# Performance work log

Measured on AMD Instinct MI355X. Metric: run time of the kernel, lower is better.

The kernel has to match this reference:

```python
import jax, jax.numpy as jnp
import numpy as np

DELTA = 0.1
NEG_INF = -1e30


def setup_inputs() -> dict:
    key = jax.random.key(0)
    k1, k2, k3, k4 = jax.random.split(key, 4)
    Bs, Bt, D, C = 8192, 8192, 64, 10
    return {
        "src_feas": jax.random.normal(k1, (Bs, D), dtype=jnp.float32),
        "src_labels": jax.random.randint(k2, (Bs,), 0, C, dtype=jnp.int32),
        "tgt_feas": jax.random.normal(k3, (Bt, D), dtype=jnp.float32),
        "tgt_logits": jax.random.normal(k4, (Bt, C), dtype=jnp.float32),
    }


def reference(src_feas, src_labels, tgt_feas, tgt_logits):
    # The original builds the explicit list of positive pairs (i_tgt, j_src)
    # where tgt sample i is 'confident' (top1-top2 logit gap >= delta) and
    # src_labels[j] == argmax(tgt_logits[i]).  The [P, P] score matrix it
    # forms is s[k, l] = src_feas[j_k] . tgt_feas[i_l], which only depends on
    # (j_k, i_l), so sum(diag(log_softmax(s))) collapses to a weighted
    # logsumexp over the [Bs, Bt] cross-domain score matrix. Same math,
    # fully vectorized, order-invariant.
    Bs = src_feas.shape[0]
    C = tgt_logits.shape[1]

    top2 = jax.lax.top_k(tgt_logits, 2)[0]                  # [Bt, 2]
    conf = (top2[:, 0] - top2[:, 1]) >= DELTA               # [Bt]
    cls = jnp.argmax(tgt_logits, axis=1)                    # [Bt]

    # per-class count of source samples
    counts = jnp.zeros((C,), jnp.float32).at[src_labels].add(1.0)  # [C]
    # w[i] = multiplicity of tgt sample i in the pair list
    w = jnp.where(conf, counts[cls], 0.0)                   # [Bt]

    M = src_feas @ tgt_feas.T                               # [Bs, Bt]
    logw = jnp.where(w > 0, jnp.log(jnp.maximum(w, 1.0)), NEG_INF)
    # L[j] = log sum over all pairs l of exp(M[j, i_l])
    L = jax.scipy.special.logsumexp(M + logw[None, :], axis=1)  # [Bs]

    pair_mask = conf[None, :] & (src_labels[:, None] == cls[None, :])  # [Bs, Bt]
    nce_sum = jnp.sum(jnp.where(pair_mask, M - L[:, None], 0.0))
    P = jnp.sum(w)                                          # total pair count
    nce = nce_sum / (-1.0 * Bs * P)
    return nce
```

## Files before the change

kernel.cpp:

```cpp
#include <hip/hip_runtime.h>
#include <hip/hip_bf16.h>

#define BSZ 8192
#define BTZ 8192
#define DD 64
#define NC 10
#define SHIFT2 20.0f
#define LN2 0.69314718055994531f
#define LOG2E 1.44269504088896341f

typedef __attribute__((ext_vector_type(8))) short bf16x8;
typedef __attribute__((ext_vector_type(4))) float f32x4;

#if defined(__has_builtin)
#if __has_builtin(__builtin_amdgcn_exp2f)
#define EXP2(x) __builtin_amdgcn_exp2f(x)
#else
#define EXP2(x) exp2f(x)
#endif
#else
#define EXP2(x) exp2f(x)
#endif

__device__ __forceinline__ unsigned short f2bf_rne(float f) {
    unsigned int u = __float_as_uint(f);
    u += 0x7FFFu + ((u >> 16) & 1u);
    return (unsigned short)(u >> 16);
}

__global__ void kA(const float4* __restrict__ src4, const float4* __restrict__ tgt4,
                   const int* __restrict__ labels,
                   ushort4* __restrict__ srcb, ushort4* __restrict__ tgtb,
                   float* __restrict__ cnt_part) {
    __shared__ float hist[NC];
    int t = threadIdx.x;
    int tid = blockIdx.x * 256 + t;
    float4 s = src4[tid];
    ushort4 os;
    os.x = f2bf_rne(s.x * LOG2E); os.y = f2bf_rne(s.y * LOG2E);
    os.z = f2bf_rne(s.z * LOG2E); os.w = f2bf_rne(s.w * LOG2E);
    srcb[tid] = os;
    float4 v = tgt4[tid];
    ushort4 ot; ot.x = f2bf_rne(v.x); ot.y = f2bf_rne(v.y);
    ot.z = f2bf_rne(v.z); ot.w = f2bf_rne(v.w);
    tgtb[tid] = ot;

    if (blockIdx.x < 32) {
        if (t < NC) hist[t] = 0.0f;
        __syncthreads();
        atomicAdd(&hist[labels[tid]], 1.0f);
        __syncthreads();
        if (t < NC) cnt_part[blockIdx.x * NC + t] = hist[t];
    }
}

__global__ void kB(const float* __restrict__ logits,
                   const float* __restrict__ cnt_part,
                   float* __restrict__ colbias, unsigned char* __restrict__ cls8,
                   float* __restrict__ cc_part, float* __restrict__ S) {
    __shared__ float lcnt[NC];
    __shared__ float hist[NC];
    int t = threadIdx.x;
    int i = blockIdx.x * 256 + t;

    if (t < NC) {
        float c = 0.0f;
        #pragma unroll
        for (int b = 0; b < 32; ++b) c += cnt_part[b * NC + t];
        lcnt[t] = c;
        hist[t] = 0.0f;
    }

    float m1 = -3.0e38f, m2 = -3.0e38f; int cls = 0;
    #pragma unroll
    for (int c = 0; c < NC; ++c) {
        float v = logits[i * NC + c];
        if (v > m1) { m2 = m1; m1 = v; cls = c; }
        else if (v > m2) { m2 = v; }
    }
    bool conf = (m1 - m2) >= 0.1f;
    __syncthreads();
    float cnt = lcnt[cls];
    bool live = conf && (cnt > 0.0f);
    colbias[i] = live ? (log2f(cnt) - SHIFT2) : -1.0e30f;
    cls8[i] = live ? (unsigned char)cls : (unsigned char)255;
    S[i] = 0.0f;
    if (conf) atomicAdd(&hist[cls], 1.0f);
    __syncthreads();
    if (t < NC) cc_part[blockIdx.x * NC + t] = hist[t];
}

__global__ __launch_bounds__(256) void kC(const unsigned short* __restrict__ srcb,
                                          const unsigned short* __restrict__ tgtb,
                                          const float* __restrict__ colbias,
                                          const unsigned char* __restrict__ cls8,
                                          const int* __restrict__ labels,
                                          float* __restrict__ S,
                                          float* __restrict__ term1_part) {
    __shared__ float lds[4][64];
    __shared__ float t1red[4];
    int t = threadIdx.x;
    int w = t >> 6;
    int lane = t & 63;
    int l15 = lane & 15;
    int quad = lane >> 4;
    int colchunk = blockIdx.x & 15;
    int rowg = blockIdx.x >> 4;
    int row_base = rowg * 64;

    bf16x8 a[4][2];
    int rl[4][4];
    #pragma unroll
    for (int mb = 0; mb < 4; ++mb) {
        const bf16x8* p = (const bf16x8*)(srcb + (size_t)(row_base + mb * 16 + l15) * DD + quad * 8);
        a[mb][0] = p[0];
        a[mb][1] = p[4];
        #pragma unroll
        for (int r = 0; r < 4; ++r)
            rl[mb][r] = labels[row_base + mb * 16 + quad * 4 + r];
    }

    float rs[4][4];
    #pragma unroll
    for (int mb = 0; mb < 4; ++mb)
        #pragma unroll
        for (int r = 0; r < 4; ++r) rs[mb][r] = 0.0f;
    float t1p = 0.0f;

    int col0 = colchunk * 512 + w * 128;
    #pragma unroll 2
    for (int ct = 0; ct < 8; ++ct) {
        int cb = col0 + ct * 16;
        const bf16x8* q = (const bf16x8*)(tgtb + (size_t)(cb + l15) * DD + quad * 8);
        bf16x8 b0 = q[0];
        bf16x8 b1 = q[4];
        float cb2 = colbias[cb + l15];
        int ccls = (int)cls8[cb + l15];
        #pragma unroll
        for (int mb = 0; mb < 4; ++mb) {
            f32x4 acc = {cb2, cb2, cb2, cb2};
            acc = __builtin_amdgcn_mfma_f32_16x16x32_bf16(a[mb][0], b0, acc, 0, 0, 0);
            acc = __builtin_amdgcn_mfma_f32_16x16x32_bf16(a[mb][1], b1, acc, 0, 0, 0);
            #pragma unroll
            for (int r = 0; r < 4; ++r) {
                float e = acc[r];
                rs[mb][r] += EXP2(e);
                t1p += (ccls == rl[mb][r]) ? (e - cb2) : 0.0f;
            }
        }
    }

    #pragma unroll
    for (int mb = 0; mb < 4; ++mb) {
        #pragma unroll
        for (int r = 0; r < 4; ++r) {
            float v = rs[mb][r];
            v += __shfl_xor(v, 1);
            v += __shfl_xor(v, 2);
            v += __shfl_xor(v, 4);
            v += __shfl_xor(v, 8);
            if (l15 == 0) lds[w][mb * 16 + quad * 4 + r] = v;
        }
    }
    float tv = t1p;
    #pragma unroll
    for (int m = 1; m < 64; m <<= 1) tv += __shfl_xor(tv, m);
    if (lane == 0) t1red[w] = tv;
    __syncthreads();
    if (t < 64)
        atomicAdd(&S[row_base + t], lds[0][t] + lds[1][t] + lds[2][t] + lds[3][t]);
    if (t == 128)
        term1_part[blockIdx.x] = t1red[0] + t1red[1] + t1red[2] + t1red[3];
}

__global__ void kD(const float* __restrict__ S, const int* __restrict__ labels,
                   const float* __restrict__ cnt_part, const float* __restrict__ cc_part,
                   const float* __restrict__ term1_part,
                   float* __restrict__ out) {
    __shared__ float counts[NC], cc[NC];
    int t = threadIdx.x;
    if (t < NC) {
        float c0 = 0.0f, c1 = 0.0f;
        #pragma unroll
        for (int b = 0; b < 32; ++b) { c0 += cnt_part[b * NC + t]; c1 += cc_part[b * NC + t]; }
        counts[t] = c0; cc[t] = c1;
    }
    __syncthreads();

    float termL = 0.0f, term1 = 0.0f, P = 0.0f;
    for (int j = t; j < BSZ; j += 256) {
        float L = (log2f(S[j]) + SHIFT2) * LN2;
        termL += cc[labels[j]] * L;
    }
    for (int o = t; o < 2048; o += 256) term1 += term1_part[o];
    if (t < NC) P = counts[t] * cc[t];

    __shared__ float redL[4], red1[4], redP[4];
    int w = t >> 6, lane = t & 63;
    float v1 = termL, v2 = term1, v3 = P;
    #pragma unroll
    for (int m = 1; m < 64; m <<= 1) {
        v1 += __shfl_xor(v1, m);
        v2 += __shfl_xor(v2, m);
        v3 += __shfl_xor(v3, m);
    }
    if (lane == 0) { redL[w] = v1; red1[w] = v2; redP[w] = v3; }
    __syncthreads();
    if (t == 0) {
        float tl = redL[0] + redL[1] + redL[2] + redL[3];
        float t1 = (red1[0] + red1[1] + red1[2] + red1[3]) * LN2;
        float p  = redP[0] + redP[1] + redP[2] + redP[3];
        out[0] = (t1 - tl) / (-(float)BSZ * p);
    }
}

extern "C" void kernel_launch(void* const* d_in, const int* in_sizes, int n_in,
                              void* d_out, int out_size, void* d_ws, size_t ws_size,
                              hipStream_t stream) {
    const float* src    = (const float*)d_in[0];
    const int*   labels = (const int*)d_in[1];
    const float* tgt    = (const float*)d_in[2];
    const float* logits = (const float*)d_in[3];

    char* ws = (char*)d_ws;
    float* S          = (float*)(ws + 0);
    float* cnt_part   = (float*)(ws + 32768);
    float* cc_part    = (float*)(ws + 34048);
    float* term1_part = (float*)(ws + 35328);
    float* colbias    = (float*)(ws + 65536);
    unsigned char* cls8 = (unsigned char*)(ws + 98304);
    unsigned short* srcb = (unsigned short*)(ws + 131072);
    unsigned short* tgtb = (unsigned short*)(ws + 131072 + 1048576);

    kA<<<512, 256, 0, stream>>>((const float4*)src, (const float4*)tgt, labels,
                                (ushort4*)srcb, (ushort4*)tgtb, cnt_part);
    kB<<<32, 256, 0, stream>>>(logits, cnt_part, colbias, cls8, cc_part, S);
    kC<<<2048, 256, 0, stream>>>(srcb, tgtb, colbias, cls8, labels, S, term1_part);
    kD<<<1, 256, 0, stream>>>(S, labels, cnt_part, cc_part, term1_part, (float*)d_out);
}
```

Before: 110.2 us.

## Compute positive-pair term via per-class target sums and fuse kernels into two

```diff
diff --git a/kernel.cpp b/kernel.cpp
--- a/kernel.cpp
+++ b/kernel.cpp
@@ -8,6 +8,7 @@
 #define SHIFT2 20.0f
 #define LN2 0.69314718055994531f
 #define LOG2E 1.44269504088896341f
+#define NEG_BIG -1.0e30f
 
 typedef __attribute__((ext_vector_type(8))) short bf16x8;
 typedef __attribute__((ext_vector_type(4))) float f32x4;
@@ -28,48 +29,51 @@
     return (unsigned short)(u >> 16);
 }
 
-__global__ void kA(const float4* __restrict__ src4, const float4* __restrict__ tgt4,
-                   const int* __restrict__ labels,
-                   ushort4* __restrict__ srcb, ushort4* __restrict__ tgtb,
-                   float* __restrict__ cnt_part) {
+__global__ __launch_bounds__(256) void kAB(const float4* __restrict__ src4,
+                                           const float4* __restrict__ tgt4,
+                                           const int* __restrict__ labels,
+                                           const float* __restrict__ logits,
+                                           const float* __restrict__ tgtf,
+                                           ushort4* __restrict__ srcb,
+                                           ushort4* __restrict__ tgtb,
+                                           float* __restrict__ S,
+                                           float* __restrict__ colbias,
+                                           float* __restrict__ cc_part,
+                                           float* __restrict__ counts_g,
+                                           float* __restrict__ accs,
+                                           int* __restrict__ ctrl,
+                                           float* __restrict__ T_part) {
     __shared__ float hist[NC];
+    __shared__ float chist[NC];
+    __shared__ unsigned char cls_l[256];
+    __shared__ float red[4 * 640];
+
     int t = threadIdx.x;
-    int tid = blockIdx.x * 256 + t;
-    float4 s = src4[tid];
-    ushort4 os;
-    os.x = f2bf_rne(s.x * LOG2E); os.y = f2bf_rne(s.y * LOG2E);
-    os.z = f2bf_rne(s.z * LOG2E); os.w = f2bf_rne(s.w * LOG2E);
-    srcb[tid] = os;
-    float4 v = tgt4[tid];
-    ushort4 ot; ot.x = f2bf_rne(v.x); ot.y = f2bf_rne(v.y);
-    ot.z = f2bf_rne(v.z); ot.w = f2bf_rne(v.w);
-    tgtb[tid] = ot;
-
-    if (blockIdx.x < 32) {
-        if (t < NC) hist[t] = 0.0f;
-        __syncthreads();
-        atomicAdd(&hist[labels[tid]], 1.0f);
-        __syncthreads();
-        if (t < NC) cnt_part[blockIdx.x * NC + t] = hist[t];
-    }
-}
-
-__global__ void kB(const float* __restrict__ logits,
-                   const float* __restrict__ cnt_part,
-                   float* __restrict__ colbias, unsigned char* __restrict__ cls8,
-                   float* __restrict__ cc_part, float* __restrict__ S) {
-    __shared__ float lcnt[NC];
-    __shared__ float hist[NC];
-    int t = threadIdx.x;
-    int i = blockIdx.x * 256 + t;
-
-    if (t < NC) {
-        float c = 0.0f;
-        #pragma unroll
-        for (int b = 0; b < 32; ++b) c += cnt_part[b * NC + t];
-        lcnt[t] = c;
-        hist[t] = 0.0f;
-    }
+    int b = blockIdx.x;
+
+    if (b < 512) {
+        int tid = b * 256 + t;
+        float4 s = src4[tid];
+        ushort4 os;
+        os.x = f2bf_rne(s.x * LOG2E); os.y = f2bf_rne(s.y * LOG2E);
+        os.z = f2bf_rne(s.z * LOG2E); os.w = f2bf_rne(s.w * LOG2E);
+        srcb[tid] = os;
+        float4 v = tgt4[tid];
+        ushort4 ot;
+        ot.x = f2bf_rne(v.x); ot.y = f2bf_rne(v.y);
+        ot.z = f2bf_rne(v.z); ot.w = f2bf_rne(v.w);
+        tgtb[tid] = ot;
+        return;
+    }
+
+    int lb = b - 512;
+    int i = lb * 256 + t;
+
+    if (t < NC) { hist[t] = 0.0f; chist[t] = 0.0f; }
+    __syncthreads();
+
+    #pragma unroll
+    for (int it = 0; it < 32; ++it) atomicAdd(&hist[labels[it * 256 + t]], 1.0f);
 
     float m1 = -3.0e38f, m2 = -3.0e38f; int cls = 0;
     #pragma unroll
@@ -80,25 +84,71 @@
     }
     bool conf = (m1 - m2) >= 0.1f;
     __syncthreads();
-    float cnt = lcnt[cls];
+
+    float cnt = hist[cls];
     bool live = conf && (cnt > 0.0f);
-    colbias[i] = live ? (log2f(cnt) - SHIFT2) : -1.0e30f;
-    cls8[i] = live ? (unsigned char)cls : (unsigned char)255;
+    colbias[i] = live ? (log2f(cnt) - SHIFT2) : NEG_BIG;
     S[i] = 0.0f;
-    if (conf) atomicAdd(&hist[cls], 1.0f);
-    __syncthreads();
-    if (t < NC) cc_part[blockIdx.x * NC + t] = hist[t];
+    cls_l[t] = live ? (unsigned char)cls : (unsigned char)255;
+    if (conf) atomicAdd(&chist[cls], 1.0f);
+    __syncthreads();
+
+    if (t < NC) cc_part[lb * NC + t] = chist[t];
+    if (lb == 0) {
+        if (t < NC) counts_g[t] = hist[t];
+        if (t < 2) accs[t] = 0.0f;
+        if (t < 129) ctrl[t] = 0;
+    }
+
+    int w = t >> 6, lane = t & 63;
+    float Ta[NC];
+    #pragma unroll
+    for (int c = 0; c < NC; ++c) Ta[c] = 0.0f;
+    int I0 = lb * 256;
+    for (int k = 0; k < 64; ++k) {
+        int li = w * 64 + k;
+        int c = (int)cls_l[li];
+        c = __builtin_amdgcn_readfirstlane(c);
+        if (c < NC) {
+            float v = tgtf[(size_t)(I0 + li) * DD + lane];
+            if      (c == 0) Ta[0] += v;
+            else if (c == 1) Ta[1] += v;
+            else if (c == 2) Ta[2] += v;
+            else if (c == 3) Ta[3] += v;
+            else if (c == 4) Ta[4] += v;
+            else if (c == 5) Ta[5] += v;
+            else if (c == 6) Ta[6] += v;
+            else if (c == 7) Ta[7] += v;
+            else if (c == 8) Ta[8] += v;
+            else             Ta[9] += v;
+        }
+    }
+    #pragma unroll
+    for (int c = 0; c < NC; ++c) red[w * 640 + c * 64 + lane] = Ta[c];
+    __syncthreads();
+    for (int idx = t; idx < 640; idx += 256)
+        T_part[lb * 640 + idx] =
+            red[idx] + red[640 + idx] + red[1280 + idx] + red[1920 + idx];
 }
 
-__global__ __launch_bounds__(256) void kC(const unsigned short* __restrict__ srcb,
-                                          const unsigned short* __restrict__ tgtb,
-                                          const float* __restrict__ colbias,
-                                          const unsigned char* __restrict__ cls8,
-                                          const int* __restrict__ labels,
-                                          float* __restrict__ S,
-                                          float* __restrict__ term1_part) {
+__global__ __launch_bounds__(256) void kCD(const unsigned short* __restrict__ srcb,
+                                           const unsigned short* __restrict__ tgtb,
+                                           const float* __restrict__ colbias,
+                                           const float* __restrict__ srcf,
+                                           const int* __restrict__ labels,
+                                           const float* __restrict__ cc_part,
+                                           const float* __restrict__ counts_g,
+                                           const float* __restrict__ T_part,
+                                           float* __restrict__ S,
+                                           float* __restrict__ accs,
+                                           int* __restrict__ ctrl,
+                                           float* __restrict__ out) {
     __shared__ float lds[4][64];
+    __shared__ float Tl[660];
     __shared__ float t1red[4];
+    __shared__ float ccl[NC];
+    __shared__ int flag1, flag2;
+
     int t = threadIdx.x;
     int w = t >> 6;
     int lane = t & 63;
@@ -109,15 +159,11 @@
     int row_base = rowg * 64;
 
     bf16x8 a[4][2];
-    int rl[4][4];
     #pragma unroll
     for (int mb = 0; mb < 4; ++mb) {
         const bf16x8* p = (const bf16x8*)(srcb + (size_t)(row_base + mb * 16 + l15) * DD + quad * 8);
         a[mb][0] = p[0];
         a[mb][1] = p[4];
-        #pragma unroll
-        for (int r = 0; r < 4; ++r)
-            rl[mb][r] = labels[row_base + mb * 16 + quad * 4 + r];
     }
 
     float rs[4][4];
@@ -125,29 +171,33 @@
     for (int mb = 0; mb < 4; ++mb)
         #pragma unroll
         for (int r = 0; r < 4; ++r) rs[mb][r] = 0.0f;
-    float t1p = 0.0f;
 
     int col0 = colchunk * 512 + w * 128;
+    const bf16x8* q0 = (const bf16x8*)(tgtb + (size_t)(col0 + l15) * DD + quad * 8);
+    bf16x8 b0 = q0[0];
+    bf16x8 b1 = q0[4];
+    float cb2 = colbias[col0 + l15];
+
     #pragma unroll 2
     for (int ct = 0; ct < 8; ++ct) {
-        int cb = col0 + ct * 16;
-        const bf16x8* q = (const bf16x8*)(tgtb + (size_t)(cb + l15) * DD + quad * 8);
-        bf16x8 b0 = q[0];
-        bf16x8 b1 = q[4];
-        float cb2 = colbias[cb + l15];
-        int ccls = (int)cls8[cb + l15];
+        bf16x8 nb0 = b0, nb1 = b1;
+        float ncb2 = cb2;
+        if (ct < 7) {
+            int cb = col0 + (ct + 1) * 16;
+            const bf16x8* qn = (const bf16x8*)(tgtb + (size_t)(cb + l15) * DD + quad * 8);
+            nb0 = qn[0];
+            nb1 = qn[4];
+            ncb2 = colbias[cb + l15];
+        }
         #pragma unroll
         for (int mb = 0; mb < 4; ++mb) {
             f32x4 acc = {cb2, cb2, cb2, cb2};
             acc = __builtin_amdgcn_mfma_f32_16x16x32_bf16(a[mb][0], b0, acc, 0, 0, 0);
             acc = __builtin_amdgcn_mfma_f32_16x16x32_bf16(a[mb][1], b1, acc, 0, 0, 0);
             #pragma unroll
-            for (int r = 0; r < 4; ++r) {
-                float e = acc[r];
-                rs[mb][r] += EXP2(e);
-                t1p += (ccls == rl[mb][r]) ? (e - cb2) : 0.0f;
-            }
-        }
+            for (int r = 0; r < 4; ++r) rs[mb][r] += EXP2(acc[r]);
+        }
+        b0 = nb0; b1 = nb1; cb2 = ncb2;
     }
 
     #pragma unroll
@@ -162,55 +212,74 @@
             if (l15 == 0) lds[w][mb * 16 + quad * 4 + r] = v;
         }
     }
-    float tv = t1p;
-    #pragma unroll
-    for (int m = 1; m < 64; m <<= 1) tv += __shfl_xor(tv, m);
-    if (lane == 0) t1red[w] = tv;
     __syncthreads();
     if (t < 64)
         atomicAdd(&S[row_base + t], lds[0][t] + lds[1][t] + lds[2][t] + lds[3][t]);
-    if (t == 128)
-        term1_part[blockIdx.x] = t1red[0] + t1red[1] + t1red[2] + t1red[3];
-}
-
-__global__ void kD(const float* __restrict__ S, const int* __restrict__ labels,
-                   const float* __restrict__ cnt_part, const float* __restrict__ cc_part,
-                   const float* __restrict__ term1_part,
-                   float* __restrict__ out) {
-    __shared__ float counts[NC], cc[NC];
-    int t = threadIdx.x;
+
+    if (colchunk == 0) {
+        for (int idx = t; idx < 640; idx += 256) {
+            float sm = 0.0f;
+            #pragma unroll
+            for (int p = 0; p < 32; ++p) sm += T_part[p * 640 + idx];
+            Tl[(idx >> 6) * 66 + (idx & 63)] = sm;
+        }
+        __syncthreads();
+        int r = t >> 2, dq = t & 3;
+        int lab = labels[row_base + r];
+        const float4* sp = (const float4*)(srcf + (size_t)(row_base + r) * DD + dq * 16);
+        float part = 0.0f;
+        #pragma unroll
+        for (int j4 = 0; j4 < 4; ++j4) {
+            float4 sv = sp[j4];
+            int tb = lab * 66 + dq * 16 + j4 * 4;
+            part += sv.x * Tl[tb] + sv.y * Tl[tb + 1] + sv.z * Tl[tb + 2] + sv.w * Tl[tb + 3];
+        }
+        #pragma unroll
+        for (int m = 1; m < 64; m <<= 1) part += __shfl_xor(part, m);
+        if (lane == 0) t1red[w] = part;
+        __syncthreads();
+        if (t == 0) atomicAdd(&accs[1], t1red[0] + t1red[1] + t1red[2] + t1red[3]);
+    }
+
+    __syncthreads();
+    __threadfence();
+    if (t == 0) { int old = atomicAdd(&ctrl[rowg], 1); flag1 = (old == 15) ? 1 : 0; }
+    __syncthreads();
+    if (!flag1) return;
+
+    __threadfence();
     if (t < NC) {
-        float c0 = 0.0f, c1 = 0.0f;
-        #pragma unroll
-        for (int b = 0; b < 32; ++b) { c0 += cnt_part[b * NC + t]; c1 += cc_part[b * NC + t]; }
-        counts[t] = c0; cc[t] = c1;
-    }
-    __syncthreads();
-
-    float termL = 0.0f, term1 = 0.0f, P = 0.0f;
-    for (int j = t; j < BSZ; j += 256) {
-        float L = (log2f(S[j]) + SHIFT2) * LN2;
-        termL += cc[labels[j]] * L;
-    }
-    for (int o = t; o < 2048; o += 256) term1 += term1_part[o];
-    if (t < NC) P = counts[t] * cc[t];
-
-    __shared__ float redL[4], red1[4], redP[4];
-    int w = t >> 6, lane = t & 63;
-    float v1 = termL, v2 = term1, v3 = P;
-    #pragma unroll
-    for (int m = 1; m < 64; m <<= 1) {
-        v1 += __shfl_xor(v1, m);
-        v2 += __shfl_xor(v2, m);
-        v3 += __shfl_xor(v3, m);
-    }
-    if (lane == 0) { redL[w] = v1; red1[w] = v2; redP[w] = v3; }
-    __syncthreads();
+        float s = 0.0f;
+        #pragma unroll
+        for (int p = 0; p < 32; ++p) s += cc_part[p * NC + t];
+        ccl[t] = s;
+    }
+    __syncthreads();
+    float val = 0.0f;
+    if (t < 64) {
+        float s = __hip_atomic_load(&S[row_base + t], __ATOMIC_RELAXED, __HIP_MEMORY_SCOPE_AGENT);
+        float L = (log2f(s) + SHIFT2) * LN2;
+        val = ccl[labels[row_base + t]] * L;
+    }
+    if (w == 0) {
+        #pragma unroll
+        for (int m = 1; m < 64; m <<= 1) val += __shfl_xor(val, m);
+        if (t == 0) atomicAdd(&accs[0], val);
+    }
     if (t == 0) {
-        float tl = redL[0] + redL[1] + redL[2] + redL[3];
-        float t1 = (red1[0] + red1[1] + red1[2] + red1[3]) * LN2;
-        float p  = redP[0] + redP[1] + redP[2] + redP[3];
-        out[0] = (t1 - tl) / (-(float)BSZ * p);
+        __threadfence();
+        int o2 = atomicAdd(&ctrl[128], 1);
+        flag2 = (o2 == 127) ? 1 : 0;
+    }
+    __syncthreads();
+    if (flag2 && t == 0) {
+        __threadfence();
+        float tl  = __hip_atomic_load(&accs[0], __ATOMIC_RELAXED, __HIP_MEMORY_SCOPE_AGENT);
+        float t1v = __hip_atomic_load(&accs[1], __ATOMIC_RELAXED, __HIP_MEMORY_SCOPE_AGENT);
+        float P = 0.0f;
+        #pragma unroll
+        for (int c = 0; c < NC; ++c) P += counts_g[c] * ccl[c];
+        out[0] = (t1v - tl) / (-(float)BSZ * P);
     }
 }
 
@@ -223,18 +292,19 @@
     const float* logits = (const float*)d_in[3];
 
     char* ws = (char*)d_ws;
-    float* S          = (float*)(ws + 0);
-    float* cnt_part   = (float*)(ws + 32768);
-    float* cc_part    = (float*)(ws + 34048);
-    float* term1_part = (float*)(ws + 35328);
-    float* colbias    = (float*)(ws + 65536);
-    unsigned char* cls8 = (unsigned char*)(ws + 98304);
-    unsigned short* srcb = (unsigned short*)(ws + 131072);
-    unsigned short* tgtb = (unsigned short*)(ws + 131072 + 1048576);
-
-    kA<<<512, 256, 0, stream>>>((const float4*)src, (const float4*)tgt, labels,
-                                (ushort4*)srcb, (ushort4*)tgtb, cnt_part);
-    kB<<<32, 256, 0, stream>>>(logits, cnt_part, colbias, cls8, cc_part, S);
-    kC<<<2048, 256, 0, stream>>>(srcb, tgtb, colbias, cls8, labels, S, term1_part);
-    kD<<<1, 256, 0, stream>>>(S, labels, cnt_part, cc_part, term1_part, (float*)d_out);
+    float* S        = (float*)(ws + 0);
+    float* colbias  = (float*)(ws + 32768);
+    float* cc_part  = (float*)(ws + 65536);
+    float* counts_g = (float*)(ws + 66816);
+    float* accs     = (float*)(ws + 66856);
+    int*   ctrl     = (int*)(ws + 66864);
+    float* T_part   = (float*)(ws + 67584);
+    unsigned short* srcb = (unsigned short*)(ws + 163840);
+    unsigned short* tgtb = (unsigned short*)(ws + 163840 + 1048576);
+
+    kAB<<<544, 256, 0, stream>>>((const float4*)src, (const float4*)tgt, labels, logits, tgt,
+                                 (ushort4*)srcb, (ushort4*)tgtb,
+                                 S, colbias, cc_part, counts_g, accs, ctrl, T_part);
+    kCD<<<2048, 256, 0, stream>>>(srcb, tgtb, colbias, src, labels,
+                                  cc_part, counts_g, T_part, S, accs, ctrl, (float*)d_out);
 }
```

Result: slower. 334.2 us (+203.1%).
